# Optimization experiments

Hardware: AMD Instinct MI355X
Metric: run time of the kernel (lower is better)

## Reference

```python
import jax, jax.numpy as jnp
import numpy as np

N_NODES = 50000
N_EDGES = 800000
IN_CH = 128
HID_CH = 128
OUT_CH = 10
NUM_GRAPHS = 128


def setup_inputs() -> dict:
    key = jax.random.key(0)
    ks = jax.random.split(key, 10)
    x = jax.random.normal(ks[0], (N_NODES, IN_CH), dtype=jnp.float32)
    edge_index = jax.random.randint(ks[1], (2, N_EDGES), 0, N_NODES, dtype=jnp.int64)
    batch = jnp.sort(jax.random.randint(ks[2], (N_NODES,), 0, NUM_GRAPHS, dtype=jnp.int64))
    s1 = 1.0 / np.sqrt(IN_CH)
    s2 = 1.0 / np.sqrt(HID_CH)
    W1 = jax.random.uniform(ks[3], (IN_CH, HID_CH), jnp.float32, -s1, s1)
    b1 = jnp.zeros((HID_CH,), jnp.float32)
    W2 = jax.random.uniform(ks[4], (HID_CH, HID_CH), jnp.float32, -s2, s2)
    b2 = jnp.zeros((HID_CH,), jnp.float32)
    Wc = jax.random.uniform(ks[5], (HID_CH, OUT_CH), jnp.float32, -s2, s2)
    bc = jax.random.uniform(ks[6], (OUT_CH,), jnp.float32, -s2, s2)
    return {"x": x, "edge_index": edge_index, "batch": batch,
            "W1": W1, "b1": b1, "W2": W2, "b2": b2, "Wc": Wc, "bc": bc}


def _gcn_norm(edge_index, num_nodes):
    # add self-loops, compute symmetric normalization deg^-1/2[src]*deg^-1/2[dst]
    loop = jnp.arange(num_nodes, dtype=edge_index.dtype)
    src = jnp.concatenate([edge_index[0], loop])
    dst = jnp.concatenate([edge_index[1], loop])
    deg = jax.ops.segment_sum(jnp.ones_like(dst, dtype=jnp.float32), dst,
                              num_segments=num_nodes)
    dinv = jnp.where(deg > 0, jax.lax.rsqrt(deg), 0.0)
    norm = dinv[src] * dinv[dst]
    return src, dst, norm


def _gcn_conv(h, src, dst, norm, W, b, num_nodes):
    h = h @ W                                    # [N, out]
    msg = h[src] * norm[:, None]                 # [E+N, out] gather + scale
    agg = jax.ops.segment_sum(msg, dst, num_segments=num_nodes)
    return agg + b


def reference(x, edge_index, batch, W1, b1, W2, b2, Wc, bc):
    n = x.shape[0]
    src, dst, norm = _gcn_norm(edge_index, n)
    h = jax.nn.relu(_gcn_conv(x, src, dst, norm, W1, b1, n))
    h = jax.nn.relu(_gcn_conv(h, src, dst, norm, W2, b2, n))
    # global mean pool over graphs
    sums = jax.ops.segment_sum(h, batch, num_segments=NUM_GRAPHS)
    cnts = jax.ops.segment_sum(jnp.ones((n,), jnp.float32), batch,
                               num_segments=NUM_GRAPHS)
    pooled = sums / jnp.maximum(cnts, 1.0)[:, None]
    # dropout is identity in eval mode
    return pooled @ Wc + bc
```

## Files before the change

### kernel.cpp

```cpp
#include <hip/hip_runtime.h>

#define N_NODES 50000
#define N_EDGES 800000
#define CH 128
#define NOUT 10
#define NUM_GRAPHS 128
#define GR 64
#define GEMM_BLOCKS ((N_NODES + GR - 1) / GR)
#define FILL_SEGS 200
#define FILL_CHUNK (N_EDGES / FILL_SEGS)
#define FILL_BLOCKS (FILL_SEGS * 8)
#define DST_RANGE (N_NODES / 8)
#define DEG_CAP 64

typedef __attribute__((ext_vector_type(8))) short bf16x8;
typedef __attribute__((ext_vector_type(4))) float f32x4;

union FragU { uint4 u; bf16x8 s; };

__device__ __forceinline__ unsigned pack_bf16(float a, float b) {
    unsigned ua = __float_as_uint(a), ub = __float_as_uint(b);
    ua += 0x7fffu + ((ua >> 16) & 1u);
    ub += 0x7fffu + ((ub >> 16) & 1u);
    return (ua >> 16) | (ub & 0xffff0000u);
}

__device__ __forceinline__ unsigned short cvt_bf16(float v) {
    unsigned u = __float_as_uint(v);
    u += 0x7fffu + ((u >> 16) & 1u);
    return (unsigned short)(u >> 16);
}

__global__ __launch_bounds__(256) void k_prep(const float* __restrict__ W1,
                                              const float* __restrict__ W2,
                                              unsigned short* __restrict__ Wb1,
                                              unsigned short* __restrict__ Wb2,
                                              int* __restrict__ fill_pos,
                                              float* __restrict__ psum) {
    if (blockIdx.x == 0) {
        for (int i = threadIdx.x; i < CH * CH; i += 256) {
            int k = i >> 7, n = i & 127;
            Wb1[((((k >> 3) << 7) + n) << 3) + (k & 7)] = cvt_bf16(W1[i]);
        }
    } else if (blockIdx.x == 1) {
        for (int i = threadIdx.x; i < CH * CH; i += 256) {
            int k = i >> 7, n = i & 127;
            int kg = k >> 3, ki = k & 7;
            int p = ((kg >> 2) << 9) + ((n & 7) << 6) + ((kg & 3) << 4) + (n >> 3);
            Wb2[(p << 3) + ki] = cvt_bf16(W2[i]);
        }
    } else if (blockIdx.x < 198) {
        int idx = (blockIdx.x - 2) * 256 + threadIdx.x;
        if (idx < N_NODES) fill_pos[idx] = 0;
    } else {
        psum[(blockIdx.x - 198) * 256 + threadIdx.x] = 0.f;
    }
}

__device__ __forceinline__ void gemm_body(const float* __restrict__ X,
                                          const unsigned short* __restrict__ Wb,
                                          unsigned short* __restrict__ Yb,
                                          int bid) {
    const int tid = threadIdx.x;
    const int w = tid >> 6;
    const int lane = tid & 63;
    const int m = lane & 15;
    const int quad = lane >> 4;
    const int row0 = bid * GR + w * 16;

    int row_a = row0 + m;
    if (row_a > N_NODES - 1) row_a = N_NODES - 1;

    const float4* Xr = (const float4*)(X + (size_t)row_a * CH) + quad * 2;
    float4 a[8];
    #pragma unroll
    for (int ks = 0; ks < 4; ++ks) {
        a[ks * 2]     = Xr[ks * 8];
        a[ks * 2 + 1] = Xr[ks * 8 + 1];
    }
    FragU af[4];
    #pragma unroll
    for (int ks = 0; ks < 4; ++ks) {
        af[ks].u.x = pack_bf16(a[ks * 2].x, a[ks * 2].y);
        af[ks].u.y = pack_bf16(a[ks * 2].z, a[ks * 2].w);
        af[ks].u.z = pack_bf16(a[ks * 2 + 1].x, a[ks * 2 + 1].y);
        af[ks].u.w = pack_bf16(a[ks * 2 + 1].z, a[ks * 2 + 1].w);
    }

    f32x4 acc[8];
    #pragma unroll
    for (int ct = 0; ct < 8; ++ct) acc[ct] = (f32x4){0.f, 0.f, 0.f, 0.f};

    const uint4* Wq = (const uint4*)Wb;
    #pragma unroll
    for (int ks = 0; ks < 4; ++ks) {
        const int kg = ks * 4 + quad;
        #pragma unroll
        for (int ct = 0; ct < 8; ++ct) {
            FragU bfu;
            bfu.u = Wq[kg * 128 + m * 8 + ct];
            acc[ct] = __builtin_amdgcn_mfma_f32_16x16x32_bf16(af[ks].s, bfu.s, acc[ct], 0, 0, 0);
        }
    }

    #pragma unroll
    for (int r = 0; r < 4; ++r) {
        int row = row0 + quad * 4 + r;
        if (row < N_NODES) {
            uint4 o;
            o.x = pack_bf16(acc[0][r], acc[1][r]);
            o.y = pack_bf16(acc[2][r], acc[3][r]);
            o.z = pack_bf16(acc[4][r], acc[5][r]);
            o.w = pack_bf16(acc[6][r], acc[7][r]);
            *(uint4*)(Yb + (size_t)row * CH + m * 8) = o;
        }
    }
}

__global__ __launch_bounds__(256) void k_gemm_fill(const float* __restrict__ X,
                                                   const unsigned short* __restrict__ Wb,
                                                   unsigned short* __restrict__ Yb,
                                                   const int* __restrict__ src,
                                                   const int* __restrict__ dst,
                                                   int* __restrict__ fill_pos,
                                                   int* __restrict__ csr_src) {
    if (blockIdx.x < GEMM_BLOCKS) {
        gemm_body(X, Wb, Yb, blockIdx.x);
    } else {
        const int b = blockIdx.x - GEMM_BLOCKS;
        const int rng = b & 7;
        const int seg = b >> 3;
        const int lo = rng * DST_RANGE, hi = lo + DST_RANGE;
        const int base = seg * FILL_CHUNK;
        for (int it = threadIdx.x * 4; it < FILL_CHUNK; it += 1024) {
            int e = base + it;
            int4 d4 = *(const int4*)(dst + e);
            int4 s4 = *(const int4*)(src + e);
            #pragma unroll
            for (int k = 0; k < 4; ++k) {
                int d = (&d4.x)[k];
                if (d >= lo && d < hi) {
                    int slot = atomicAdd(&fill_pos[d], 1);
                    if (slot < DEG_CAP) csr_src[(d << 6) + slot] = (&s4.x)[k];
                }
            }
        }
    }
}

__device__ __forceinline__ void acc_row(float (&x)[8], uint4 q, float w) {
    #pragma unroll
    for (int t = 0; t < 4; ++t) {
        unsigned r = ((const unsigned*)&q)[t];
        x[2 * t]     = fmaf(w, __uint_as_float(r << 16), x[2 * t]);
        x[2 * t + 1] = fmaf(w, __uint_as_float(r & 0xffff0000u), x[2 * t + 1]);
    }
}

__global__ __launch_bounds__(256) void k_gather_w2(const unsigned* __restrict__ tb,
                                                   const int* __restrict__ csr_src,
                                                   const int* __restrict__ cnt,
                                                   const float* __restrict__ bias,
                                                   const unsigned short* __restrict__ Wb,
                                                   unsigned short* __restrict__ tb2) {
    const int wid = threadIdx.x >> 6;
    const int lane = threadIdx.x & 63;
    const int sub = lane >> 4;
    const int cidx = lane & 15;
    const int v = blockIdx.x * 4 + wid;

    int lenc = cnt[v];
    const float dv = rsqrtf((float)(lenc + 1));
    int len = lenc > DEG_CAP ? DEG_CAP : lenc;

    int u_l = 0;
    float w_l = 0.f;
    if (lane < len) {
        u_l = csr_src[(v << 6) + lane];
        w_l = rsqrtf((float)(cnt[u_l] + 1));
    }

    const uint4* tbq = (const uint4*)tb;
    float x[8];
    #pragma unroll
    for (int t = 0; t < 8; ++t) x[t] = 0.f;

    const int ng = (len + 3) >> 2;
    for (int g = 0; g < ng; g += 8) {
        uint4 q[8];
        float w[8];
        #pragma unroll
        for (int k = 0; k < 8; ++k) {
            if (g + k < ng) {
                int idx = (g + k) * 4 + sub;
                bool act = idx < len;
                int ic = act ? idx : 0;
                int u = __shfl(u_l, ic);
                w[k] = act ? __shfl(w_l, ic) : 0.f;
                q[k] = tbq[(size_t)u * 16 + cidx];
            }
        }
        #pragma unroll
        for (int k = 0; k < 8; ++k)
            if (g + k < ng) acc_row(x, q[k], w[k]);
    }
    {
        uint4 q = tbq[(size_t)v * 16 + cidx];
        float w = (sub == 0) ? dv : 0.f;
        acc_row(x, q, w);
    }
    #pragma unroll
    for (int t = 0; t < 8; ++t) {
        x[t] += __shfl_xor(x[t], 16);
        x[t] += __shfl_xor(x[t], 32);
    }

    const float4* b4 = (const float4*)bias;
    float4 b0 = b4[cidx * 2], b1v = b4[cidx * 2 + 1];
    unsigned pk[4];
    pk[0] = pack_bf16(fmaxf(fmaf(dv, x[0], b0.x), 0.f),
                      fmaxf(fmaf(dv, x[1], b0.y), 0.f));
    pk[1] = pack_bf16(fmaxf(fmaf(dv, x[2], b0.z), 0.f),
                      fmaxf(fmaf(dv, x[3], b0.w), 0.f));
    pk[2] = pack_bf16(fmaxf(fmaf(dv, x[4], b1v.x), 0.f),
                      fmaxf(fmaf(dv, x[5], b1v.y), 0.f));
    pk[3] = pack_bf16(fmaxf(fmaf(dv, x[6], b1v.z), 0.f),
                      fmaxf(fmaf(dv, x[7], b1v.w), 0.f));

    f32x4 acc[8];
    #pragma unroll
    for (int ct = 0; ct < 8; ++ct) acc[ct] = (f32x4){0.f, 0.f, 0.f, 0.f};
    const uint4* Wq = (const uint4*)Wb;
    #pragma unroll
    for (int ks = 0; ks < 4; ++ks) {
        const int hl = ks * 4 + sub;
        FragU af;
        af.u.x = __shfl(pk[0], hl);
        af.u.y = __shfl(pk[1], hl);
        af.u.z = __shfl(pk[2], hl);
        af.u.w = __shfl(pk[3], hl);
        #pragma unroll
        for (int ct = 0; ct < 8; ++ct) {
            FragU bfu;
            bfu.u = Wq[(ks << 9) + (ct << 6) + lane];
            acc[ct] = __builtin_amdgcn_mfma_f32_16x16x32_bf16(af.s, bfu.s, acc[ct], 0, 0, 0);
        }
    }
    if (sub == 0) {
        uint4 o;
        o.x = pack_bf16(acc[0][0] * dv, acc[1][0] * dv);
        o.y = pack_bf16(acc[2][0] * dv, acc[3][0] * dv);
        o.z = pack_bf16(acc[4][0] * dv, acc[5][0] * dv);
        o.w = pack_bf16(acc[6][0] * dv, acc[7][0] * dv);
        *(uint4*)(tb2 + (size_t)v * CH + cidx * 8) = o;
    }
}

__global__ __launch_bounds__(256) void k_gather_pool(const unsigned* __restrict__ tb,
                                                     const int* __restrict__ csr_src,
                                                     const int* __restrict__ cnt,
                                                     const float* __restrict__ bias,
                                                     const int* __restrict__ batch,
                                                     float* __restrict__ psum) {
    const int wid = threadIdx.x >> 6;
    const int lane = threadIdx.x & 63;
    const int sub = lane >> 4;
    const int cidx = lane & 15;
    const int v = blockIdx.x * 4 + wid;

    int lenc = cnt[v];
    const float dv = rsqrtf((float)(lenc + 1));
    int len = lenc > DEG_CAP ? DEG_CAP : lenc;

    int u_l = 0;
    if (lane < len) u_l = csr_src[(v << 6) + lane];

    const uint4* tbq = (const uint4*)tb;
    float x[8];
    #pragma unroll
    for (int t = 0; t < 8; ++t) x[t] = 0.f;

    const int ng = (len + 3) >> 2;
    for (int g = 0; g < ng; g += 8) {
        uint4 q[8];
        float w[8];
        #pragma unroll
        for (int k = 0; k < 8; ++k) {
            if (g + k < ng) {
                int idx = (g + k) * 4 + sub;
                bool act = idx < len;
                int ic = act ? idx : 0;
                int u = __shfl(u_l, ic);
                w[k] = act ? 1.f : 0.f;
                q[k] = tbq[(size_t)u * 16 + cidx];
            }
        }
        #pragma unroll
        for (int k = 0; k < 8; ++k)
            if (g + k < ng) acc_row(x, q[k], w[k]);
    }
    {
        uint4 q = tbq[(size_t)v * 16 + cidx];
        float w = (sub == 0) ? 1.f : 0.f;
        acc_row(x, q, w);
    }
    #pragma unroll
    for (int t = 0; t < 8; ++t) {
        x[t] += __shfl_xor(x[t], 16);
        x[t] += __shfl_xor(x[t], 32);
    }

    const float4* b4 = (const float4*)bias;
    float4 b0 = b4[cidx * 2], b1 = b4[cidx * 2 + 1];
    float o[8];
    o[0] = fmaxf(fmaf(dv, x[0], b0.x), 0.f);
    o[1] = fmaxf(fmaf(dv, x[1], b0.y), 0.f);
    o[2] = fmaxf(fmaf(dv, x[2], b0.z), 0.f);
    o[3] = fmaxf(fmaf(dv, x[3], b0.w), 0.f);
    o[4] = fmaxf(fmaf(dv, x[4], b1.x), 0.f);
    o[5] = fmaxf(fmaf(dv, x[5], b1.y), 0.f);
    o[6] = fmaxf(fmaf(dv, x[6], b1.z), 0.f);
    o[7] = fmaxf(fmaf(dv, x[7], b1.w), 0.f);

    __shared__ float sh[4][128];
    __shared__ int sg[4];
    if (lane == 0) sg[wid] = batch[v];
    if (sub == 0) {
        float4* shp = (float4*)&sh[wid][cidx * 8];
        shp[0] = (float4){o[0], o[1], o[2], o[3]};
        shp[1] = (float4){o[4], o[5], o[6], o[7]};
    }
    __syncthreads();
    const int tid = threadIdx.x;
    if (tid < 128) {
        int g0 = sg[0], g1 = sg[1], g2 = sg[2], g3 = sg[3];
        float v0 = sh[0][tid], v1 = sh[1][tid], v2 = sh[2][tid], v3 = sh[3][tid];
        if (g0 == g3) {
            atomicAdd(&psum[g0 * CH + tid], v0 + v1 + v2 + v3);
        } else {
            if (g0 == g1) v1 += v0; else atomicAdd(&psum[g0 * CH + tid], v0);
            if (g1 == g2) v2 += v1; else atomicAdd(&psum[g1 * CH + tid], v1);
            if (g2 == g3) v3 += v2; else atomicAdd(&psum[g2 * CH + tid], v2);
            atomicAdd(&psum[g3 * CH + tid], v3);
        }
    }
}

__global__ __launch_bounds__(128) void k_classify(const float* __restrict__ psum,
                                                  const int* __restrict__ batch,
                                                  const float* __restrict__ Wc,
                                                  const float* __restrict__ bc,
                                                  float* __restrict__ out) {
    __shared__ float p[CH];
    __shared__ float sinv;
    int g = blockIdx.x;
    int tid = threadIdx.x;
    if (tid == 0) {
        int lo = 0, hi = N_NODES;
        while (lo < hi) { int mid = (lo + hi) >> 1; if (batch[mid] < g) lo = mid + 1; else hi = mid; }
        int start = lo;
        lo = 0; hi = N_NODES;
        while (lo < hi) { int mid = (lo + hi) >> 1; if (batch[mid] < g + 1) lo = mid + 1; else hi = mid; }
        sinv = 1.0f / fmaxf((float)(lo - start), 1.0f);
    }
    __syncthreads();
    p[tid] = psum[g * CH + tid] * sinv;
    __syncthreads();
    if (tid < NOUT) {
        float acc = bc[tid];
        #pragma unroll 4
        for (int k = 0; k < CH; ++k) acc += p[k] * Wc[k * NOUT + tid];
        out[g * NOUT + tid] = acc;
    }
}

extern "C" void kernel_launch(void* const* d_in, const int* in_sizes, int n_in,
                              void* d_out, int out_size, void* d_ws, size_t ws_size,
                              hipStream_t stream) {
    const float* x     = (const float*)d_in[0];
    const int*   ei    = (const int*)d_in[1];
    const int*   batch = (const int*)d_in[2];
    const float* W1    = (const float*)d_in[3];
    const float* b1    = (const float*)d_in[4];
    const float* W2    = (const float*)d_in[5];
    const float* b2    = (const float*)d_in[6];
    const float* Wc    = (const float*)d_in[7];
    const float* bc    = (const float*)d_in[8];
    float* out = (float*)d_out;

    const int* src = ei;
    const int* dst = ei + N_EDGES;

    int*            fill_pos = (int*)d_ws;
    int*            csr_src  = fill_pos + N_NODES;
    unsigned short* wb1      = (unsigned short*)(csr_src + (size_t)N_NODES * DEG_CAP);
    unsigned short* wb2      = wb1 + CH * CH;
    unsigned short* tb       = wb2 + CH * CH;
    unsigned short* tb2      = tb + (size_t)N_NODES * CH;
    float*          psum     = (float*)(tb2 + (size_t)N_NODES * CH);

    k_prep<<<198 + 64, 256, 0, stream>>>(W1, W2, wb1, wb2, fill_pos, psum);

    k_gemm_fill<<<GEMM_BLOCKS + FILL_BLOCKS, 256, 0, stream>>>(
        x, wb1, tb, src, dst, fill_pos, csr_src);

    k_gather_w2<<<N_NODES / 4, 256, 0, stream>>>((unsigned*)tb, csr_src, fill_pos, b1,
                                                 wb2, tb2);

    k_gather_pool<<<N_NODES / 4, 256, 0, stream>>>((unsigned*)tb2, csr_src, fill_pos, b2,
                                                   batch, psum);

    k_classify<<<NUM_GRAPHS, 128, 0, stream>>>(psum, batch, Wc, bc, out);
}
```

Baseline: 279.8 us.

## Split each node's gather across two waves, each handling half the channels

The two gather kernels now assign two wavefronts per node, each covering 64 of the 128 channels, with 8 neighbours processed per pass instead of 4. All neighbour row loads are issued up front in a single unrolled batch, which raises memory-level parallelism and halves the per-wave latency chain. The W2 MFMA stage is split so each half-wave computes four output column tiles, staging the bf16 activations through shared memory instead of lane shuffles. It doubles the block count and adds a block-wide barrier and an extra shuffle-reduction stage. The pool path pairs two nodes per block for its atomic adds.

```diff
diff --git a/kernel.cpp b/kernel.cpp
--- a/kernel.cpp
+++ b/kernel.cpp
@@ -157,103 +157,146 @@
     }
 }
 
+template <bool W2>
+__device__ __forceinline__ void gather8_body(const uint4* __restrict__ tbq,
+                                             const int* __restrict__ csr_src,
+                                             const int* __restrict__ cnt,
+                                             const float* __restrict__ bias,
+                                             const unsigned short* __restrict__ Wb,
+                                             unsigned short* __restrict__ tb2,
+                                             const int* __restrict__ batch,
+                                             float* __restrict__ psum) {
+    const int tid = threadIdx.x;
+    const int wid = tid >> 6;
+    const int lane = tid & 63;
+    const int nib = wid >> 1;
+    const int half = wid & 1;
+    const int sub = lane >> 3;
+    const int cidx = lane & 7;
+    const int v = blockIdx.x * 2 + nib;
+
+    int lenc = cnt[v];
+    const float dv = rsqrtf((float)(lenc + 1));
+    int len = lenc > DEG_CAP ? DEG_CAP : lenc;
+
+    int u_l = 0;
+    float w_l = 0.f;
+    if (lane < len) {
+        u_l = csr_src[(v << 6) + lane];
+        if (W2) w_l = rsqrtf((float)(cnt[u_l] + 1));
+    }
+
+    const int nb = (len + 7) >> 3;
+    uint4 q[8];
+    float w[8];
+    #pragma unroll
+    for (int k = 0; k < 8; ++k) {
+        if (k < nb) {
+            int ridx = k * 8 + sub;
+            bool act = ridx < len;
+            int ic = act ? ridx : 0;
+            int u = __shfl(u_l, ic);
+            float ws = W2 ? __shfl(w_l, ic) : 1.f;
+            w[k] = act ? ws : 0.f;
+            q[k] = tbq[(size_t)u * 16 + half * 8 + cidx];
+        }
+    }
+    uint4 qs = tbq[(size_t)v * 16 + half * 8 + cidx];
+
+    float x[8];
+    #pragma unroll
+    for (int t = 0; t < 8; ++t) x[t] = 0.f;
+    #pragma unroll
+    for (int k = 0; k < 8; ++k)
+        if (k < nb) acc_row(x, q[k], w[k]);
+    acc_row(x, qs, (sub == 0) ? (W2 ? dv : 1.f) : 0.f);
+
+    #pragma unroll
+    for (int t = 0; t < 8; ++t) {
+        x[t] += __shfl_xor(x[t], 8);
+        x[t] += __shfl_xor(x[t], 16);
+        x[t] += __shfl_xor(x[t], 32);
+    }
+
+    const float4* b4 = (const float4*)bias;
+    float4 b0 = b4[half * 16 + cidx * 2], b1v = b4[half * 16 + cidx * 2 + 1];
+    float o[8];
+    o[0] = fmaxf(fmaf(dv, x[0], b0.x), 0.f);
+    o[1] = fmaxf(fmaf(dv, x[1], b0.y), 0.f);
+    o[2] = fmaxf(fmaf(dv, x[2], b0.z), 0.f);
+    o[3] = fmaxf(fmaf(dv, x[3], b0.w), 0.f);
+    o[4] = fmaxf(fmaf(dv, x[4], b1v.x), 0.f);
+    o[5] = fmaxf(fmaf(dv, x[5], b1v.y), 0.f);
+    o[6] = fmaxf(fmaf(dv, x[6], b1v.z), 0.f);
+    o[7] = fmaxf(fmaf(dv, x[7], b1v.w), 0.f);
+
+    if constexpr (W2) {
+        __shared__ uint4 shh[2][16];
+        if (sub == 0) {
+            uint4 pkv;
+            pkv.x = pack_bf16(o[0], o[1]);
+            pkv.y = pack_bf16(o[2], o[3]);
+            pkv.z = pack_bf16(o[4], o[5]);
+            pkv.w = pack_bf16(o[6], o[7]);
+            shh[nib][half * 8 + cidx] = pkv;
+        }
+        __syncthreads();
+
+        const int quad = lane >> 4;
+        const int m = lane & 15;
+        FragU af[4];
+        #pragma unroll
+        for (int ks = 0; ks < 4; ++ks) af[ks].u = shh[nib][ks * 4 + quad];
+
+        f32x4 acc[4];
+        #pragma unroll
+        for (int j = 0; j < 4; ++j) acc[j] = (f32x4){0.f, 0.f, 0.f, 0.f};
+        const uint4* Wq = (const uint4*)Wb;
+        #pragma unroll
+        for (int ks = 0; ks < 4; ++ks) {
+            #pragma unroll
+            for (int j = 0; j < 4; ++j) {
+                FragU bfu;
+                bfu.u = Wq[(ks << 9) + ((half * 4 + j) << 6) + lane];
+                acc[j] = __builtin_amdgcn_mfma_f32_16x16x32_bf16(af[ks].s, bfu.s, acc[j], 0, 0, 0);
+            }
+        }
+        if (quad == 0) {
+            uint2 ov;
+            ov.x = pack_bf16(acc[0][0] * dv, acc[1][0] * dv);
+            ov.y = pack_bf16(acc[2][0] * dv, acc[3][0] * dv);
+            *(uint2*)(tb2 + (size_t)v * CH + m * 8 + half * 4) = ov;
+        }
+    } else {
+        __shared__ float sh[2][128];
+        __shared__ int sg[2];
+        if (lane == 0 && half == 0) sg[nib] = batch[v];
+        if (sub == 0) {
+            float4* shp = (float4*)&sh[nib][half * 64 + cidx * 8];
+            shp[0] = (float4){o[0], o[1], o[2], o[3]};
+            shp[1] = (float4){o[4], o[5], o[6], o[7]};
+        }
+        __syncthreads();
+        if (tid < 128) {
+            int g0 = sg[0], g1 = sg[1];
+            float v0 = sh[0][tid], v1 = sh[1][tid];
+            if (g0 == g1) {
+                atomicAdd(&psum[g0 * CH + tid], v0 + v1);
+            } else {
+                atomicAdd(&psum[g0 * CH + tid], v0);
+                atomicAdd(&psum[g1 * CH + tid], v1);
+            }
+        }
+    }
+}
+
 __global__ __launch_bounds__(256) void k_gather_w2(const unsigned* __restrict__ tb,
                                                    const int* __restrict__ csr_src,
                                                    const int* __restrict__ cnt,
                                                    const float* __restrict__ bias,
                                                    const unsigned short* __restrict__ Wb,
                                                    unsigned short* __restrict__ tb2) {
-    const int wid = threadIdx.x >> 6;
-    const int lane = threadIdx.x & 63;
-    const int sub = lane >> 4;
-    const int cidx = lane & 15;
-    const int v = blockIdx.x * 4 + wid;
-
-    int lenc = cnt[v];
-    const float dv = rsqrtf((float)(lenc + 1));
-    int len = lenc > DEG_CAP ? DEG_CAP : lenc;
-
-    int u_l = 0;
-    float w_l = 0.f;
-    if (lane < len) {
-        u_l = csr_src[(v << 6) + lane];
-        w_l = rsqrtf((float)(cnt[u_l] + 1));
-    }
-
-    const uint4* tbq = (const uint4*)tb;
-    float x[8];
-    #pragma unroll
-    for (int t = 0; t < 8; ++t) x[t] = 0.f;
-
-    const int ng = (len + 3) >> 2;
-    for (int g = 0; g < ng; g += 8) {
-        uint4 q[8];
-        float w[8];
-        #pragma unroll
-        for (int k = 0; k < 8; ++k) {
-            if (g + k < ng) {
-                int idx = (g + k) * 4 + sub;
-                bool act = idx < len;
-                int ic = act ? idx : 0;
-                int u = __shfl(u_l, ic);
-                w[k] = act ? __shfl(w_l, ic) : 0.f;
-                q[k] = tbq[(size_t)u * 16 + cidx];
-            }
-        }
-        #pragma unroll
-        for (int k = 0; k < 8; ++k)
-            if (g + k < ng) acc_row(x, q[k], w[k]);
-    }
-    {
-        uint4 q = tbq[(size_t)v * 16 + cidx];
-        float w = (sub == 0) ? dv : 0.f;
-        acc_row(x, q, w);
-    }
-    #pragma unroll
-    for (int t = 0; t < 8; ++t) {
-        x[t] += __shfl_xor(x[t], 16);
-        x[t] += __shfl_xor(x[t], 32);
-    }
-
-    const float4* b4 = (const float4*)bias;
-    float4 b0 = b4[cidx * 2], b1v = b4[cidx * 2 + 1];
-    unsigned pk[4];
-    pk[0] = pack_bf16(fmaxf(fmaf(dv, x[0], b0.x), 0.f),
-                      fmaxf(fmaf(dv, x[1], b0.y), 0.f));
-    pk[1] = pack_bf16(fmaxf(fmaf(dv, x[2], b0.z), 0.f),
-                      fmaxf(fmaf(dv, x[3], b0.w), 0.f));
-    pk[2] = pack_bf16(fmaxf(fmaf(dv, x[4], b1v.x), 0.f),
-                      fmaxf(fmaf(dv, x[5], b1v.y), 0.f));
-    pk[3] = pack_bf16(fmaxf(fmaf(dv, x[6], b1v.z), 0.f),
-                      fmaxf(fmaf(dv, x[7], b1v.w), 0.f));
-
-    f32x4 acc[8];
-    #pragma unroll
-    for (int ct = 0; ct < 8; ++ct) acc[ct] = (f32x4){0.f, 0.f, 0.f, 0.f};
-    const uint4* Wq = (const uint4*)Wb;
-    #pragma unroll
-    for (int ks = 0; ks < 4; ++ks) {
-        const int hl = ks * 4 + sub;
-        FragU af;
-        af.u.x = __shfl(pk[0], hl);
-        af.u.y = __shfl(pk[1], hl);
-        af.u.z = __shfl(pk[2], hl);
-        af.u.w = __shfl(pk[3], hl);
-        #pragma unroll
-        for (int ct = 0; ct < 8; ++ct) {
-            FragU bfu;
-            bfu.u = Wq[(ks << 9) + (ct << 6) + lane];
-            acc[ct] = __builtin_amdgcn_mfma_f32_16x16x32_bf16(af.s, bfu.s, acc[ct], 0, 0, 0);
-        }
-    }
-    if (sub == 0) {
-        uint4 o;
-        o.x = pack_bf16(acc[0][0] * dv, acc[1][0] * dv);
-        o.y = pack_bf16(acc[2][0] * dv, acc[3][0] * dv);
-        o.z = pack_bf16(acc[4][0] * dv, acc[5][0] * dv);
-        o.w = pack_bf16(acc[6][0] * dv, acc[7][0] * dv);
-        *(uint4*)(tb2 + (size_t)v * CH + cidx * 8) = o;
-    }
+    gather8_body<true>((const uint4*)tb, csr_src, cnt, bias, Wb, tb2, nullptr, nullptr);
 }
 
 __global__ __launch_bounds__(256) void k_gather_pool(const unsigned* __restrict__ tb,
@@ -262,88 +305,7 @@
                                                      const float* __restrict__ bias,
                                                      const int* __restrict__ batch,
                                                      float* __restrict__ psum) {
-    const int wid = threadIdx.x >> 6;
-    const int lane = threadIdx.x & 63;
-    const int sub = lane >> 4;
-    const int cidx = lane & 15;
-    const int v = blockIdx.x * 4 + wid;
-
-    int lenc = cnt[v];
-    const float dv = rsqrtf((float)(lenc + 1));
-    int len = lenc > DEG_CAP ? DEG_CAP : lenc;
-
-    int u_l = 0;
-    if (lane < len) u_l = csr_src[(v << 6) + lane];
-
-    const uint4* tbq = (const uint4*)tb;
-    float x[8];
-    #pragma unroll
-    for (int t = 0; t < 8; ++t) x[t] = 0.f;
-
-    const int ng = (len + 3) >> 2;
-    for (int g = 0; g < ng; g += 8) {
-        uint4 q[8];
-        float w[8];
-        #pragma unroll
-        for (int k = 0; k < 8; ++k) {
-            if (g + k < ng) {
-                int idx = (g + k) * 4 + sub;
-                bool act = idx < len;
-                int ic = act ? idx : 0;
-                int u = __shfl(u_l, ic);
-                w[k] = act ? 1.f : 0.f;
-                q[k] = tbq[(size_t)u * 16 + cidx];
-            }
-        }
-        #pragma unroll
-        for (int k = 0; k < 8; ++k)
-            if (g + k < ng) acc_row(x, q[k], w[k]);
-    }
-    {
-        uint4 q = tbq[(size_t)v * 16 + cidx];
-        float w = (sub == 0) ? 1.f : 0.f;
-        acc_row(x, q, w);
-    }
-    #pragma unroll
-    for (int t = 0; t < 8; ++t) {
-        x[t] += __shfl_xor(x[t], 16);
-        x[t] += __shfl_xor(x[t], 32);
-    }
-
-    const float4* b4 = (const float4*)bias;
-    float4 b0 = b4[cidx * 2], b1 = b4[cidx * 2 + 1];
-    float o[8];
-    o[0] = fmaxf(fmaf(dv, x[0], b0.x), 0.f);
-    o[1] = fmaxf(fmaf(dv, x[1], b0.y), 0.f);
-    o[2] = fmaxf(fmaf(dv, x[2], b0.z), 0.f);
-    o[3] = fmaxf(fmaf(dv, x[3], b0.w), 0.f);
-    o[4] = fmaxf(fmaf(dv, x[4], b1.x), 0.f);
-    o[5] = fmaxf(fmaf(dv, x[5], b1.y), 0.f);
-    o[6] = fmaxf(fmaf(dv, x[6], b1.z), 0.f);
-    o[7] = fmaxf(fmaf(dv, x[7], b1.w), 0.f);
-
-    __shared__ float sh[4][128];
-    __shared__ int sg[4];
-    if (lane == 0) sg[wid] = batch[v];
-    if (sub == 0) {
-        float4* shp = (float4*)&sh[wid][cidx * 8];
-        shp[0] = (float4){o[0], o[1], o[2], o[3]};
-        shp[1] = (float4){o[4], o[5], o[6], o[7]};
-    }
-    __syncthreads();
-    const int tid = threadIdx.x;
-    if (tid < 128) {
-        int g0 = sg[0], g1 = sg[1], g2 = sg[2], g3 = sg[3];
-        float v0 = sh[0][tid], v1 = sh[1][tid], v2 = sh[2][tid], v3 = sh[3][tid];
-        if (g0 == g3) {
-            atomicAdd(&psum[g0 * CH + tid], v0 + v1 + v2 + v3);
-        } else {
-            if (g0 == g1) v1 += v0; else atomicAdd(&psum[g0 * CH + tid], v0);
-            if (g1 == g2) v2 += v1; else atomicAdd(&psum[g1 * CH + tid], v1);
-            if (g2 == g3) v3 += v2; else atomicAdd(&psum[g2 * CH + tid], v2);
-            atomicAdd(&psum[g3 * CH + tid], v3);
-        }
-    }
+    gather8_body<false>((const uint4*)tb, csr_src, cnt, bias, nullptr, nullptr, batch, psum);
 }
 
 __global__ __launch_bounds__(128) void k_classify(const float* __restrict__ psum,
@@ -404,10 +366,10 @@
     k_gemm_fill<<<GEMM_BLOCKS + FILL_BLOCKS, 256, 0, stream>>>(
         x, wb1, tb, src, dst, fill_pos, csr_src);
 
-    k_gather_w2<<<N_NODES / 4, 256, 0, stream>>>((unsigned*)tb, csr_src, fill_pos, b1,
+    k_gather_w2<<<N_NODES / 2, 256, 0, stream>>>((unsigned*)tb, csr_src, fill_pos, b1,
                                                  wb2, tb2);
 
-    k_gather_pool<<<N_NODES / 4, 256, 0, stream>>>((unsigned*)tb2, csr_src, fill_pos, b2,
+    k_gather_pool<<<N_NODES / 2, 256, 0, stream>>>((unsigned*)tb2, csr_src, fill_pos, b2,
                                                    batch, psum);
 
     k_classify<<<NUM_GRAPHS, 128, 0, stream>>>(psum, batch, Wc, bc, out);
```

New measurement: 311.0 us. 1.11x slower.
